# Kernel optimization log

Hardware: AMD Instinct MI355X
Metric: run time of the kernel (lower is better)

Reference implementation:

```python
import jax, jax.numpy as jnp
import numpy as np

C = 256
D = C // 8  # query/key channels
B, H, W = 4, 64, 64


def setup_inputs() -> dict:
    key = jax.random.key(0)
    ks = jax.random.split(key, 9)
    s = 0.02
    return {
        "z": jax.random.normal(ks[0], (B, C, H, W), jnp.float32),
        "x": jax.random.normal(ks[1], (B, C, H, W), jnp.float32),
        "y": jax.random.normal(ks[2], (B, C, H, W), jnp.float32),
        "Wq": jax.random.normal(ks[3], (D, C), jnp.float32) * s,
        "bq": jnp.zeros((D,), jnp.float32),
        "Wk": jax.random.normal(ks[4], (D, C), jnp.float32) * s,
        "bk": jnp.zeros((D,), jnp.float32),
        "Wv": jax.random.normal(ks[5], (C, C), jnp.float32) * s,
        "bv": jnp.zeros((C,), jnp.float32),
    }


def reference(z, x, y, Wq, bq, Wk, bk, Wv, bv):
    b, c, h, w = x.shape
    n = h * w
    xf = x.reshape(b, c, n)  # [B,C,N]
    yf = y.reshape(b, c, n)
    zf = z.reshape(b, c, n)
    # 1x1 convs == channel-wise linear projections
    q = jnp.einsum("dc,bcn->bnd", Wq, xf) + bq                 # [B,N,D]
    k = jnp.einsum("dc,bcn->bdn", Wk, yf) + bk[:, None]        # [B,D,N]
    energy = jnp.einsum("bnd,bdm->bnm", q, k)                  # [B,N,N]
    attn = jax.nn.softmax(energy, axis=-1)                     # rows over keys
    v = jnp.einsum("ec,bcn->ben", Wv, zf) + bv[:, None]        # [B,C,N]
    # torch: bmm(value, attn^T) -> out[b,c,m] = sum_n v[b,c,n]*attn[b,m,n]
    out = jnp.einsum("ben,bmn->bem", v, attn)                  # [B,C,N]
    return z + out.reshape(b, c, h, w)
```

## Files before the change

kernel.cpp:

```cpp
#include <hip/hip_runtime.h>
#include <hip/hip_bf16.h>

#define Bn 4
#define Cn 256
#define Dn 32
#define Nn 4096

typedef __attribute__((ext_vector_type(8))) short short8;
typedef __attribute__((ext_vector_type(4))) float f32x4;

union U16 { uint4 u; short8 s; };

__device__ __forceinline__ unsigned short f2bf(float f) {
  union { __hip_bfloat16 h; unsigned short u; } c;
  c.h = __float2bfloat16(f);
  return c.u;
}

__global__ __launch_bounds__(640, 1) void SA_proj2(
    const float* __restrict__ x, const float* __restrict__ y, const float* __restrict__ z,
    const float* __restrict__ Wq, const float* __restrict__ bq,
    const float* __restrict__ Wk, const float* __restrict__ bk,
    const float* __restrict__ Wv, const float* __restrict__ bv,
    unsigned short* __restrict__ qws, unsigned short* __restrict__ kws,
    unsigned short* __restrict__ vws)
{
  __shared__ char lds[3 * 33280];
  const int bid = blockIdx.x, tid = threadIdx.x;
  const int lane = tid & 63, wv2 = tid >> 6;
  const int g = lane >> 4, l15 = lane & 15;
  const int b = bid >> 6, n0 = (bid & 63) << 6;
  const int kt = n0 >> 6;

  const float* src0 = x + (size_t)b * Cn * Nn;
  const float* src1 = y + (size_t)b * Cn * Nn;
  const float* src2 = z + (size_t)b * Cn * Nn;

  const int isv = (wv2 >= 2);
  const float* W    = isv ? Wv : (wv2 == 0 ? Wq : Wk);
  const float* bias = isv ? bv : (wv2 == 0 ? bq : bk);
  const int e0w = isv ? ((wv2 - 2) << 5) : 0;
  const char* myT = lds + (isv ? 2 : wv2) * 33280;

  const int cl = tid >> 2, fq = tid & 3;

  f32x4 sl0[4], sl1[4], sl2[4];
  auto stage_ld = [&](int ck) {
    const size_t row = (size_t)(ck * 128 + cl) * Nn + n0 + fq * 4;
#pragma unroll
    for (int i = 0; i < 4; ++i) sl0[i] = *(const f32x4*)(src0 + row + i * 16);
#pragma unroll
    for (int i = 0; i < 4; ++i) sl1[i] = *(const f32x4*)(src1 + row + i * 16);
#pragma unroll
    for (int i = 0; i < 4; ++i) sl2[i] = *(const f32x4*)(src2 + row + i * 16);
  };
  auto stage_wr = [&](int ck) {
    const int cb = (ck * 128 + cl) * 2;
#pragma unroll
    for (int i = 0; i < 4; ++i)
#pragma unroll
      for (int j = 0; j < 4; ++j) {
        char* rp = lds + (size_t)(fq * 4 + i * 16 + j) * 520 + cb;
        *(unsigned short*)(rp)         = f2bf(sl0[i][j]);
        *(unsigned short*)(rp + 33280) = f2bf(sl1[i][j]);
        *(unsigned short*)(rp + 66560) = f2bf(sl2[i][j]);
      }
  };

  f32x4 wf[2][4][2];
  auto w_ld = [&](int ck) {
#pragma unroll
    for (int et = 0; et < 2; ++et) {
      const float* wp = W + (size_t)(e0w + 16 * et + l15) * 256 + ck * 128 + 4 * g;
#pragma unroll
      for (int cc = 0; cc < 4; ++cc) {
        wf[et][cc][0] = *(const f32x4*)(wp + cc * 32);
        wf[et][cc][1] = *(const f32x4*)(wp + cc * 32 + 16);
      }
    }
  };
  short8 af[2][4];
  auto w_cvt = [&]() {
#pragma unroll
    for (int et = 0; et < 2; ++et)
#pragma unroll
      for (int cc = 0; cc < 4; ++cc) {
        short8 t8;
#pragma unroll
        for (int j = 0; j < 4; ++j) {
          t8[j]     = (short)f2bf(wf[et][cc][0][j]);
          t8[4 + j] = (short)f2bf(wf[et][cc][1][j]);
        }
        af[et][cc] = t8;
      }
  };

  f32x4 acc[2][4];
#pragma unroll
  for (int et = 0; et < 2; ++et)
#pragma unroll
    for (int ns = 0; ns < 4; ++ns) { acc[et][ns][0]=0.f; acc[et][ns][1]=0.f; acc[et][ns][2]=0.f; acc[et][ns][3]=0.f; }

  auto compute = [&](int ck) {
#pragma unroll
    for (int cc = 0; cc < 4; ++cc) {
      const int cbyte = (ck * 128 + cc * 32 + 4 * g) * 2;
#pragma unroll
      for (int ns = 0; ns < 4; ++ns) {
        const char* rp = myT + (size_t)(16 * ns + l15) * 520 + cbyte;
        U16 bb;
        bb.u.x = *(const unsigned*)rp;        bb.u.y = *(const unsigned*)(rp + 4);
        bb.u.z = *(const unsigned*)(rp + 32); bb.u.w = *(const unsigned*)(rp + 36);
#pragma unroll
        for (int et = 0; et < 2; ++et)
          acc[et][ns] = __builtin_amdgcn_mfma_f32_16x16x32_bf16(af[et][cc], bb.s, acc[et][ns], 0, 0, 0);
      }
    }
  };

  if (tid < 512) stage_ld(0);
  w_ld(0);
  if (tid < 512) stage_wr(0);
  __syncthreads();
  w_cvt();
  if (tid < 512) stage_ld(1);
  compute(0);
  if (tid < 512) stage_wr(1);
  w_ld(1);
  __syncthreads();
  w_cvt();
  compute(1);
  __syncthreads();

  float bvv[2][4];
#pragma unroll
  for (int et = 0; et < 2; ++et)
#pragma unroll
    for (int r = 0; r < 4; ++r) bvv[et][r] = bias[e0w + 16 * et + 4 * g + r];

  if (isv) {
    const int vw = wv2 - 2, Wt = vw >> 1, w1 = vw & 1;
#pragma unroll
    for (int et = 0; et < 2; ++et)
#pragma unroll
      for (int ns = 0; ns < 4; ++ns)
#pragma unroll
        for (int r = 0; r < 4; ++r) {
          int byte = Wt * 8192 + (((2 * w1 + et) << 1) + (ns >> 1)) * 1024
                   + ((l15 >> 2) * 16 + 4 * g + r) * 16 + (ns & 1) * 8 + (l15 & 3) * 2;
          *(unsigned short*)(lds + byte) = f2bf(acc[et][ns][r] + bvv[et][r]);
        }
  } else if (wv2 == 0) {
    char* base = lds + 66560;
#pragma unroll
    for (int et = 0; et < 2; ++et)
#pragma unroll
      for (int ns = 0; ns < 4; ++ns)
#pragma unroll
        for (int r = 0; r < 4; ++r) {
          int d = 16 * et + 4 * g + r;
          int n = 16 * ns + l15;
          *(unsigned short*)(base + (size_t)n * 80 + d * 2) = f2bf(acc[et][ns][r] + bvv[et][r]);
        }
  } else {
    char* base = lds + 71680;
#pragma unroll
    for (int et = 0; et < 2; ++et)
#pragma unroll
      for (int ns = 0; ns < 4; ++ns)
#pragma unroll
        for (int r = 0; r < 4; ++r) {
          int pos = ns * 1024 + g * 256 + l15 * 16 + et * 8 + r * 2;
          *(unsigned short*)(base + pos) = f2bf(acc[et][ns][r] + bvv[et][r]);
        }
  }
  __syncthreads();

  if (tid < 512) {
    char* gb = (char*)vws + (size_t)b * Cn * Nn * 2 + (size_t)kt * 32768 + tid * 64;
    const char* lb = lds + tid * 64;
#pragma unroll
    for (int i = 0; i < 4; ++i)
      *(uint4*)(gb + i * 16) = *(const uint4*)(lb + i * 16);
  }
  if (wv2 == 0) {
    unsigned short* ob = qws + (size_t)b * Nn * Dn;
#pragma unroll
    for (int i = 0; i < 4; ++i) {
      int flat = 64 * i + lane;
      *(uint4*)((char*)ob + (size_t)n0 * 64 + flat * 16)
          = *(const uint4*)(lds + 66560 + (size_t)(flat >> 2) * 80 + (flat & 3) * 16);
    }
  } else if (wv2 == 1) {
    char* ob = (char*)kws + (size_t)b * Nn * Dn * 2 + (size_t)kt * 4096;
#pragma unroll
    for (int i = 0; i < 4; ++i) {
      int flat = 64 * i + lane;
      *(uint4*)(ob + flat * 16) = *(const uint4*)(lds + 71680 + flat * 16);
    }
  }
}

__global__ __launch_bounds__(512, 2) void SA_flash(
    const unsigned short* __restrict__ qws, const unsigned short* __restrict__ kws,
    const unsigned short* __restrict__ vws, const float* __restrict__ z,
    float* __restrict__ outp)
{
  __shared__ char lds[68608];
  float*    m_arr = (float*)(lds + 66560);
  float*    l_arr = (float*)(lds + 67072);
  float*    a_arr = (float*)(lds + 67584);
  unsigned* f_arr = (unsigned*)(lds + 68096);

  const int bid = blockIdx.x;
  const int b    = (bid >> 1) & 3;
  const int mblk = ((bid >> 3) << 1) | (bid & 1);
  const int m0 = mblk * 64;
  const int tid = threadIdx.x, lane = tid & 63;
  const int wv = tid >> 6, gg = wv >> 2, wq = wv & 3;
  const int g = lane >> 4, l15 = lane & 15;

  char* Pg = lds + gg * 8192;

  const unsigned short* qb = qws + (size_t)b * Nn * Dn;
  const char* kb = (const char*)kws + (size_t)b * Nn * Dn * 2;
  const char* vb = (const char*)vws + (size_t)b * Cn * Nn * 2;

  const int mw = m0 + 16 * wq;
  short8 qf;
  {
    const char* qp = (const char*)qb + (size_t)(mw + l15) * 64 + 8 * g;
    ushort4 q0 = *(const ushort4*)qp;
    ushort4 q1 = *(const ushort4*)(qp + 32);
    qf[0]=(short)q0.x; qf[1]=(short)q0.y; qf[2]=(short)q0.z; qf[3]=(short)q0.w;
    qf[4]=(short)q1.x; qf[5]=(short)q1.y; qf[6]=(short)q1.z; qf[7]=(short)q1.w;
  }

  f32x4 acc[4][4];
#pragma unroll
  for (int et = 0; et < 4; ++et)
#pragma unroll
    for (int qt = 0; qt < 4; ++qt) { acc[et][qt][0]=0.f; acc[et][qt][1]=0.f; acc[et][qt][2]=0.f; acc[et][qt][3]=0.f; }
  float m_run = -__builtin_inff(), l_run = 0.f;

  uint4 kfr[4], vfr[8];
  auto k_ld = [&](int t4) {
    const char* p = kb + (size_t)t4 * 4096 + lane * 16;
#pragma unroll
    for (int t = 0; t < 4; ++t) kfr[t] = *(const uint4*)(p + t * 1024);
  };
  auto v_ld = [&](int t4) {
    const char* p = vb + (size_t)t4 * 32768 + wq * 8192 + lane * 16;
#pragma unroll
    for (int f = 0; f < 8; ++f) vfr[f] = *(const uint4*)(p + f * 1024);
  };
  k_ld(gg); v_ld(gg);

  for (int it = 0; it < 32; ++it) {
    f32x4 s[4];
    const f32x4 zero4 = {0.f, 0.f, 0.f, 0.f};
#pragma unroll
    for (int t = 0; t < 4; ++t) {
      U16 ku; ku.u = kfr[t];
      s[t] = __builtin_amdgcn_mfma_f32_16x16x32_bf16(ku.s, qf, zero4, 0, 0, 0);
    }
    if (it < 31) k_ld(2 * (it + 1) + gg);

    float pm = s[0][0];
#pragma unroll
    for (int t = 0; t < 4; ++t)
#pragma unroll
      for (int r = 0; r < 4; ++r) pm = fmaxf(pm, s[t][r]);
    pm = fmaxf(pm, __shfl_xor(pm, 16, 64));
    pm = fmaxf(pm, __shfl_xor(pm, 32, 64));
    int trig = __any(pm > m_run);
    float alpha = 1.0f;
    if (trig) {
      float mn = fmaxf(m_run, pm);
      alpha = __expf(m_run - mn);
      l_run *= alpha;
      m_run = mn;
    }
    float p[4][4]; float rs = 0.f;
#pragma unroll
    for (int t = 0; t < 4; ++t)
#pragma unroll
      for (int r = 0; r < 4; ++r) { float e = __expf(s[t][r] - m_run); p[t][r] = e; rs += e; }
    rs += __shfl_xor(rs, 16, 64);
    rs += __shfl_xor(rs, 32, 64);
    l_run += rs;

    short8 pf[2];
#pragma unroll
    for (int c = 0; c < 2; ++c) {
      short8 t8;
      t8[0]=(short)f2bf(p[2*c][0]);   t8[1]=(short)f2bf(p[2*c][1]);
      t8[2]=(short)f2bf(p[2*c][2]);   t8[3]=(short)f2bf(p[2*c][3]);
      t8[4]=(short)f2bf(p[2*c+1][0]); t8[5]=(short)f2bf(p[2*c+1][1]);
      t8[6]=(short)f2bf(p[2*c+1][2]); t8[7]=(short)f2bf(p[2*c+1][3]);
      pf[c] = t8;
    }
    *(short8*)(Pg + (wq * 2 + 0) * 1024 + lane * 16) = pf[0];
    *(short8*)(Pg + (wq * 2 + 1) * 1024 + lane * 16) = pf[1];
    if (lane < 16) a_arr[gg * 64 + 16 * wq + lane] = alpha;
    if (lane == 0) f_arr[gg * 4 + wq] = (unsigned)trig;
    __syncthreads();

    {
      uint4 fl = *(const uint4*)(f_arr + gg * 4);
      if (fl.x | fl.y | fl.z | fl.w) {
        float al4[4];
#pragma unroll
        for (int qt = 0; qt < 4; ++qt) al4[qt] = a_arr[gg * 64 + 16 * qt + l15];
#pragma unroll
        for (int et = 0; et < 4; ++et)
#pragma unroll
          for (int qt = 0; qt < 4; ++qt) {
            acc[et][qt][0]*=al4[qt]; acc[et][qt][1]*=al4[qt];
            acc[et][qt][2]*=al4[qt]; acc[et][qt][3]*=al4[qt];
          }
      }
    }

    __builtin_amdgcn_s_setprio(1);
#pragma unroll
    for (int qt = 0; qt < 4; ++qt) {
#pragma unroll
      for (int ks = 0; ks < 2; ++ks) {
        short8 pfr = *(const short8*)(Pg + (qt * 2 + ks) * 1024 + lane * 16);
#pragma unroll
        for (int et = 0; et < 4; ++et) {
          U16 vu; vu.u = vfr[et * 2 + ks];
          acc[et][qt] = __builtin_amdgcn_mfma_f32_16x16x32_bf16(vu.s, pfr, acc[et][qt], 0, 0, 0);
        }
      }
    }
    __builtin_amdgcn_s_setprio(0);
    if (it < 31) v_ld(2 * (it + 1) + gg);
    __syncthreads();
  }

  if (lane < 16) {
    m_arr[gg * 64 + 16 * wq + lane] = m_run;
    l_arr[gg * 64 + 16 * wq + lane] = l_run;
  }
  __syncthreads();
  float fmy[4], inv[4];
#pragma unroll
  for (int qt = 0; qt < 4; ++qt) {
    int q = 16 * qt + l15;
    float mv0 = m_arr[q], mv1 = m_arr[64 + q];
    float lv0 = l_arr[q], lv1 = l_arr[64 + q];
    float M = fmaxf(mv0, mv1);
    float f0 = __expf(mv0 - M), f1 = __expf(mv1 - M);
    inv[qt] = 1.0f / (lv0 * f0 + lv1 * f1);
    fmy[qt] = gg ? f1 : f0;
  }
#pragma unroll
  for (int et = 0; et < 4; ++et)
#pragma unroll
    for (int qt = 0; qt < 4; ++qt) {
      acc[et][qt][0]*=fmy[qt]; acc[et][qt][1]*=fmy[qt];
      acc[et][qt][2]*=fmy[qt]; acc[et][qt][3]*=fmy[qt];
    }
  if (gg == 1) {
#pragma unroll
    for (int et = 0; et < 4; ++et)
#pragma unroll
      for (int qt = 0; qt < 4; ++qt)
        *(f32x4*)(lds + (size_t)(16 * qt + l15) * 1040 + (64 * wq + 16 * et + 4 * g) * 4) = acc[et][qt];
  }
  __syncthreads();
  if (gg == 0) {
    const float* zb = z    + (size_t)b * Cn * Nn;
    float*       ob = outp + (size_t)b * Cn * Nn;
#pragma unroll
    for (int et = 0; et < 4; ++et)
#pragma unroll
      for (int qt = 0; qt < 4; ++qt) {
        f32x4 o = *(const f32x4*)(lds + (size_t)(16 * qt + l15) * 1040 + (64 * wq + 16 * et + 4 * g) * 4);
        int q = m0 + 16 * qt + l15;
#pragma unroll
        for (int r = 0; r < 4; ++r) {
          int e = 64 * wq + 16 * et + 4 * g + r;
          size_t off = (size_t)e * Nn + q;
          ob[off] = zb[off] + (acc[et][qt][r] + o[r]) * inv[qt];
        }
      }
  }
}

extern "C" void kernel_launch(void* const* d_in, const int* in_sizes, int n_in,
                              void* d_out, int out_size, void* d_ws, size_t ws_size,
                              hipStream_t stream) {
  (void)in_sizes; (void)n_in; (void)out_size; (void)ws_size;
  const float* z  = (const float*)d_in[0];
  const float* x  = (const float*)d_in[1];
  const float* y  = (const float*)d_in[2];
  const float* Wq = (const float*)d_in[3];
  const float* bq = (const float*)d_in[4];
  const float* Wk = (const float*)d_in[5];
  const float* bk = (const float*)d_in[6];
  const float* Wv = (const float*)d_in[7];
  const float* bv = (const float*)d_in[8];
  float* out = (float*)d_out;

  unsigned short* qws = (unsigned short*)d_ws;
  unsigned short* kws = qws + (size_t)Bn * Nn * Dn;
  unsigned short* vws = kws + (size_t)Bn * Nn * Dn;

  SA_proj2<<<256, 640, 0, stream>>>(x, y, z, Wq, bq, Wk, bk, Wv, bv, qws, kws, vws);
  SA_flash<<<256, 512, 0, stream>>>(qws, kws, vws, z, out);
}
```

Baseline: 172.4 us.

## Double-buffer P tiles to overlap softmax with previous PV MFMA

Restructures the flash loop into a skewed software pipeline. Each iteration first runs the P·V MFMAs for the previous key tile, then computes QK scores and softmax for the current tile, writing P, alpha and the trigger flags into alternating LDS slots. This cuts the two workgroup barriers per iteration down to one and lets exponent work overlap the matrix work of the previous tile. In exchange it uses more LDS, and the V fragment loads are now issued only one stage before their use.

```diff
diff --git a/kernel.cpp b/kernel.cpp
--- a/kernel.cpp
+++ b/kernel.cpp
@@ -206,11 +206,11 @@
     const unsigned short* __restrict__ vws, const float* __restrict__ z,
     float* __restrict__ outp)
 {
-  __shared__ char lds[68608];
+  __shared__ char lds[69760];
   float*    m_arr = (float*)(lds + 66560);
   float*    l_arr = (float*)(lds + 67072);
   float*    a_arr = (float*)(lds + 67584);
-  unsigned* f_arr = (unsigned*)(lds + 68096);
+  unsigned* f_arr = (unsigned*)(lds + 69632);
 
   const int bid = blockIdx.x;
   const int b    = (bid >> 1) & 3;
@@ -220,7 +220,7 @@
   const int wv = tid >> 6, gg = wv >> 2, wq = wv & 3;
   const int g = lane >> 4, l15 = lane & 15;
 
-  char* Pg = lds + gg * 8192;
+  char* Pg = lds + gg * 16384;
 
   const unsigned short* qb = qws + (size_t)b * Nn * Dn;
   const char* kb = (const char*)kws + (size_t)b * Nn * Dn * 2;
@@ -254,64 +254,16 @@
 #pragma unroll
     for (int f = 0; f < 8; ++f) vfr[f] = *(const uint4*)(p + f * 1024);
   };
-  k_ld(gg); v_ld(gg);
-
-  for (int it = 0; it < 32; ++it) {
-    f32x4 s[4];
-    const f32x4 zero4 = {0.f, 0.f, 0.f, 0.f};
-#pragma unroll
-    for (int t = 0; t < 4; ++t) {
-      U16 ku; ku.u = kfr[t];
-      s[t] = __builtin_amdgcn_mfma_f32_16x16x32_bf16(ku.s, qf, zero4, 0, 0, 0);
-    }
-    if (it < 31) k_ld(2 * (it + 1) + gg);
-
-    float pm = s[0][0];
-#pragma unroll
-    for (int t = 0; t < 4; ++t)
-#pragma unroll
-      for (int r = 0; r < 4; ++r) pm = fmaxf(pm, s[t][r]);
-    pm = fmaxf(pm, __shfl_xor(pm, 16, 64));
-    pm = fmaxf(pm, __shfl_xor(pm, 32, 64));
-    int trig = __any(pm > m_run);
-    float alpha = 1.0f;
-    if (trig) {
-      float mn = fmaxf(m_run, pm);
-      alpha = __expf(m_run - mn);
-      l_run *= alpha;
-      m_run = mn;
-    }
-    float p[4][4]; float rs = 0.f;
-#pragma unroll
-    for (int t = 0; t < 4; ++t)
-#pragma unroll
-      for (int r = 0; r < 4; ++r) { float e = __expf(s[t][r] - m_run); p[t][r] = e; rs += e; }
-    rs += __shfl_xor(rs, 16, 64);
-    rs += __shfl_xor(rs, 32, 64);
-    l_run += rs;
-
-    short8 pf[2];
-#pragma unroll
-    for (int c = 0; c < 2; ++c) {
-      short8 t8;
-      t8[0]=(short)f2bf(p[2*c][0]);   t8[1]=(short)f2bf(p[2*c][1]);
-      t8[2]=(short)f2bf(p[2*c][2]);   t8[3]=(short)f2bf(p[2*c][3]);
-      t8[4]=(short)f2bf(p[2*c+1][0]); t8[5]=(short)f2bf(p[2*c+1][1]);
-      t8[6]=(short)f2bf(p[2*c+1][2]); t8[7]=(short)f2bf(p[2*c+1][3]);
-      pf[c] = t8;
-    }
-    *(short8*)(Pg + (wq * 2 + 0) * 1024 + lane * 16) = pf[0];
-    *(short8*)(Pg + (wq * 2 + 1) * 1024 + lane * 16) = pf[1];
-    if (lane < 16) a_arr[gg * 64 + 16 * wq + lane] = alpha;
-    if (lane == 0) f_arr[gg * 4 + wq] = (unsigned)trig;
-    __syncthreads();
-
-    {
-      uint4 fl = *(const uint4*)(f_arr + gg * 4);
+  k_ld(gg);
+
+  for (int it = 0; it < 33; ++it) {
+    if (it > 0) {
+      const int sl = (it - 1) & 1;
+      uint4 fl = *(const uint4*)(f_arr + sl * 8 + gg * 4);
       if (fl.x | fl.y | fl.z | fl.w) {
         float al4[4];
 #pragma unroll
-        for (int qt = 0; qt < 4; ++qt) al4[qt] = a_arr[gg * 64 + 16 * qt + l15];
+        for (int qt = 0; qt < 4; ++qt) al4[qt] = a_arr[sl * 128 + gg * 64 + 16 * qt + l15];
 #pragma unroll
         for (int et = 0; et < 4; ++et)
 #pragma unroll
@@ -320,24 +272,75 @@
             acc[et][qt][2]*=al4[qt]; acc[et][qt][3]*=al4[qt];
           }
       }
-    }
-
-    __builtin_amdgcn_s_setprio(1);
-#pragma unroll
-    for (int qt = 0; qt < 4; ++qt) {
-#pragma unroll
-      for (int ks = 0; ks < 2; ++ks) {
-        short8 pfr = *(const short8*)(Pg + (qt * 2 + ks) * 1024 + lane * 16);
-#pragma unroll
-        for (int et = 0; et < 4; ++et) {
-          U16 vu; vu.u = vfr[et * 2 + ks];
-          acc[et][qt] = __builtin_amdgcn_mfma_f32_16x16x32_bf16(vu.s, pfr, acc[et][qt], 0, 0, 0);
-        }
-      }
-    }
-    __builtin_amdgcn_s_setprio(0);
-    if (it < 31) v_ld(2 * (it + 1) + gg);
-    __syncthreads();
+      __builtin_amdgcn_s_setprio(1);
+#pragma unroll
+      for (int qt = 0; qt < 4; ++qt) {
+#pragma unroll
+        for (int ks = 0; ks < 2; ++ks) {
+          short8 pfr = *(const short8*)(Pg + sl * 8192 + (qt * 2 + ks) * 1024 + lane * 16);
+#pragma unroll
+          for (int et = 0; et < 4; ++et) {
+            U16 vu; vu.u = vfr[et * 2 + ks];
+            acc[et][qt] = __builtin_amdgcn_mfma_f32_16x16x32_bf16(vu.s, pfr, acc[et][qt], 0, 0, 0);
+          }
+        }
+      }
+      __builtin_amdgcn_s_setprio(0);
+    }
+    if (it < 32) {
+      v_ld(2 * it + gg);
+      f32x4 s[4];
+      const f32x4 zero4 = {0.f, 0.f, 0.f, 0.f};
+#pragma unroll
+      for (int t = 0; t < 4; ++t) {
+        U16 ku; ku.u = kfr[t];
+        s[t] = __builtin_amdgcn_mfma_f32_16x16x32_bf16(ku.s, qf, zero4, 0, 0, 0);
+      }
+      if (it < 31) k_ld(2 * (it + 1) + gg);
+
+      float pm = s[0][0];
+#pragma unroll
+      for (int t = 0; t < 4; ++t)
+#pragma unroll
+        for (int r = 0; r < 4; ++r) pm = fmaxf(pm, s[t][r]);
+      pm = fmaxf(pm, __shfl_xor(pm, 16, 64));
+      pm = fmaxf(pm, __shfl_xor(pm, 32, 64));
+      int trig = __any(pm > m_run);
+      float alpha = 1.0f;
+      if (trig) {
+        float mn = fmaxf(m_run, pm);
+        alpha = __expf(m_run - mn);
+        l_run *= alpha;
+        m_run = mn;
+      }
+      float p[4][4]; float rs = 0.f;
+#pragma unroll
+      for (int t = 0; t < 4; ++t)
+#pragma unroll
+        for (int r = 0; r < 4; ++r) { float e = __expf(s[t][r] - m_run); p[t][r] = e; rs += e; }
+      rs += __shfl_xor(rs, 16, 64);
+      rs += __shfl_xor(rs, 32, 64);
+      l_run += rs;
+
+      short8 pf0, pf1;
+      pf0[0]=(short)f2bf(p[0][0]); pf0[1]=(short)f2bf(p[0][1]);
+      pf0[2]=(short)f2bf(p[0][2]); pf0[3]=(short)f2bf(p[0][3]);
+      pf0[4]=(short)f2bf(p[1][0]); pf0[5]=(short)f2bf(p[1][1]);
+      pf0[6]=(short)f2bf(p[1][2]); pf0[7]=(short)f2bf(p[1][3]);
+      pf1[0]=(short)f2bf(p[2][0]); pf1[1]=(short)f2bf(p[2][1]);
+      pf1[2]=(short)f2bf(p[2][2]); pf1[3]=(short)f2bf(p[2][3]);
+      pf1[4]=(short)f2bf(p[3][0]); pf1[5]=(short)f2bf(p[3][1]);
+      pf1[6]=(short)f2bf(p[3][2]); pf1[7]=(short)f2bf(p[3][3]);
+      const int sw = it & 1;
+      *(short8*)(Pg + sw * 8192 + (wq * 2 + 0) * 1024 + lane * 16) = pf0;
+      *(short8*)(Pg + sw * 8192 + (wq * 2 + 1) * 1024 + lane * 16) = pf1;
+      if (lane < 16) a_arr[sw * 128 + gg * 64 + 16 * wq + lane] = alpha;
+      if (lane == 0) f_arr[sw * 8 + gg * 4 + wq] = (unsigned)trig;
+
+      asm volatile("s_waitcnt lgkmcnt(0)" ::: "memory");
+      __builtin_amdgcn_s_barrier();
+      __builtin_amdgcn_sched_barrier(0);
+    }
   }
 
   if (lane < 16) {
```

Result: no change. 170.7 us (-1.0%).
